# Kernel tuning notes

Measured on AMD Instinct MI355X. Metric: run time of the kernel, lower is better.

Reference implementation:

```python
import jax, jax.numpy as jnp
import numpy as np

B, S, D = 16, 4096, 1024
DIM_K, DIM_V, NUM_HEAD = 1024, 1024, 16


def setup_inputs() -> dict:
    key = jax.random.key(0)
    ks = jax.random.split(key, 7)
    s_in = 1.0 / np.sqrt(D)
    return {
        "x": jax.random.normal(ks[0], (B, S, D), dtype=jnp.float32),
        "Wq": jax.random.normal(ks[1], (D, DIM_K), dtype=jnp.float32) * s_in,
        "bq": jnp.zeros((DIM_K,), dtype=jnp.float32),
        "Wk": jax.random.normal(ks[2], (D, DIM_K), dtype=jnp.float32) * s_in,
        "bk": jnp.zeros((DIM_K,), dtype=jnp.float32),
        "Wv": jax.random.normal(ks[3], (D, DIM_V), dtype=jnp.float32) * s_in,
        "bv": jnp.zeros((DIM_V,), dtype=jnp.float32),
    }


def reference(x, Wq, bq, Wk, bk, Wv, bv):
    H = NUM_HEAD
    b, s, _ = x.shape
    Q = x @ Wq + bq                      # (B,S,dim_k)
    K = x @ Wk + bk                      # (B,S,dim_k)
    V = x @ Wv + bv                      # (B,S,dim_v)
    Q_ = Q.reshape(b, s, H, DIM_K // H)  # (B,S,H,dk)
    K_ = K.reshape(b, s, H, DIM_K // H)
    V_ = V.reshape(b, s, H, DIM_V // H)
    # NOTE: faithful to the source quirk — scores are across HEADS (H x H)
    # at each (batch, seq) position; no 1/sqrt(dim_k) scaling (unused in source).
    scores = jnp.einsum("bshd,bsgd->bshg", Q_, K_)   # (B,S,H,H)
    atten = jax.nn.softmax(scores, axis=-1)
    out = jnp.einsum("bshg,bsgd->bshd", atten, V_)    # (B,S,H,dv_head)
    return out.reshape(b, s, -1)                      # (B,S,dim_v)
```

## Files before the change

kernel.cpp:

```cpp
#include <hip/hip_runtime.h>
#include <stdint.h>

#define M_TOTAL 65536
#define DIM     1024
#define NQKV    3072
#define NHEAD   16
#define HDIM    64

typedef __attribute__((ext_vector_type(8))) _Float16 f16x8;
typedef __attribute__((ext_vector_type(4))) _Float16 f16x4;
typedef __attribute__((ext_vector_type(4))) float    f32x4;

__global__ __launch_bounds__(256) void cvt_x_kernel(const float* __restrict__ x,
                                                    _Float16* __restrict__ xh,
                                                    int n4) {
    int i = blockIdx.x * blockDim.x + threadIdx.x;
    int stride = gridDim.x * blockDim.x;
    const float4* x4 = (const float4*)x;
    f16x4* o4 = (f16x4*)xh;
    for (; i < n4; i += stride) {
        float4 v = x4[i];
        f16x4 o;
        o[0] = (_Float16)v.x; o[1] = (_Float16)v.y;
        o[2] = (_Float16)v.z; o[3] = (_Float16)v.w;
        o4[i] = o;
    }
}

__global__ void cvt_w_kernel(const float* __restrict__ Wq,
                             const float* __restrict__ Wk,
                             const float* __restrict__ Wv,
                             _Float16* __restrict__ Wt) {
    __shared__ float tile[32][33];
    int which = blockIdx.z;
    const float* W = (which == 0) ? Wq : (which == 1) ? Wk : Wv;
    int d0 = blockIdx.y * 32, n0 = blockIdx.x * 32;
    int tx = threadIdx.x, ty = threadIdx.y;
    tile[ty][tx] = W[(size_t)(d0 + ty) * DIM + n0 + tx];
    __syncthreads();
    Wt[(size_t)(which * DIM + n0 + ty) * DIM + d0 + tx] = (_Float16)tile[tx][ty];
}

__global__ __launch_bounds__(256) void bias_kernel(const float* __restrict__ bq,
                                                   const float* __restrict__ bk,
                                                   const float* __restrict__ bv,
                                                   float* __restrict__ bias) {
    int i = blockIdx.x * 256 + threadIdx.x;
    if (i < NQKV)
        bias[i] = (i < 1024) ? bq[i] : (i < 2048) ? bk[i - 1024] : bv[i - 2048];
}


#define LDSA(slot)  ((slot) << 15)
#define LDSB(slot)  (65536 + ((slot) << 15))

__global__ __launch_bounds__(512, 2) void qkv_gemm_kernel(const _Float16* __restrict__ Xh,
                                                          const _Float16* __restrict__ Wth,
                                                          const float* __restrict__ bias,
                                                          _Float16* __restrict__ Ch) {
    extern __shared__ char smem[];

    const int bid = blockIdx.x;
    const int swz = (bid & 7) * (3072 / 8) + (bid >> 3);
    const int tm  = swz / (NQKV / 256);
    const int tn  = swz % (NQKV / 256);
    const int brow = tm * 256;
    const int bcol = tn * 256;

    const int tid = threadIdx.x;
    const int w   = tid >> 6;
    const int l   = tid & 63;
    const int wm  = w >> 2;
    const int wn  = w & 3;

    const int lrow8 = l >> 3;
    const int lcol8 = (l & 7) ^ lrow8;
    const _Float16* pAsrc = Xh  + (size_t)(brow + w * 8 + lrow8) * DIM + lcol8 * 8;
    const _Float16* pBsrc = Wth + (size_t)(bcol + w * 8 + lrow8) * DIM + lcol8 * 8;

    auto stageA = [&](int slot, int kt) {
#pragma unroll
        for (int ln = 0; ln < 4; ++ln) {
            const _Float16* s = pAsrc + (size_t)(ln * 64) * DIM + ((size_t)kt << 6);
            char* d = smem + LDSA(slot) + ln * 8192 + (w << 10);
            __builtin_amdgcn_global_load_lds((const __attribute__((address_space(1))) void*)s,
                                             (__attribute__((address_space(3))) void*)d, 16, 0, 0);
        }
    };
    auto stageB = [&](int slot, int kt) {
#pragma unroll
        for (int ln = 0; ln < 4; ++ln) {
            const _Float16* s = pBsrc + (size_t)(ln * 64) * DIM + ((size_t)kt << 6);
            char* d = smem + LDSB(slot) + ln * 8192 + (w << 10);
            __builtin_amdgcn_global_load_lds((const __attribute__((address_space(1))) void*)s,
                                             (__attribute__((address_space(3))) void*)d, 16, 0, 0);
        }
    };

    const int aRowB = ((wm << 7) + (l & 15)) << 7;
    const int bRowB = 65536 + (((wn << 6) + (l & 15)) << 7);
    const int xk0 = (((l >> 4) ^ (l & 7)) << 4);
    const int xk1 = ((((l >> 4) + 4) ^ (l & 7)) << 4);
    auto LDA = [&](int slot, int mi, int ks) -> f16x8 {
        return *(const f16x8*)(smem + (slot << 15) + aRowB + (mi << 11) + (ks ? xk1 : xk0));
    };
    auto LDB = [&](int slot, int ni, int ks) -> f16x8 {
        return *(const f16x8*)(smem + (slot << 15) + bRowB + (ni << 11) + (ks ? xk1 : xk0));
    };

    f32x4 acc[8][4] = {};
    f16x8 a[8][2], b[4][2];

    auto READS = [&](int slot) {
#pragma unroll
        for (int mi = 0; mi < 8; ++mi) { a[mi][0] = LDA(slot, mi, 0); a[mi][1] = LDA(slot, mi, 1); }
#pragma unroll
        for (int ni = 0; ni < 4; ++ni) { b[ni][0] = LDB(slot, ni, 0); b[ni][1] = LDB(slot, ni, 1); }
    };

    stageA(0, 0); stageB(0, 0);
    stageA(1, 1); stageB(1, 1);
    asm volatile("s_waitcnt vmcnt(8)" ::: "memory");
    __builtin_amdgcn_s_barrier();
    __builtin_amdgcn_sched_barrier(0);
    READS(0);

#pragma unroll 1
    for (int u = 0; u < 16; ++u) {
        const int s = u & 1;

        __builtin_amdgcn_s_setprio(1);
#pragma unroll
        for (int mi = 0; mi < 8; ++mi)
#pragma unroll
            for (int ni = 0; ni < 4; ++ni) {
                acc[mi][ni] = __builtin_amdgcn_mfma_f32_16x16x32_f16(b[ni][0], a[mi][0], acc[mi][ni], 0, 0, 0);
                acc[mi][ni] = __builtin_amdgcn_mfma_f32_16x16x32_f16(b[ni][1], a[mi][1], acc[mi][ni], 0, 0, 0);
            }
        __builtin_amdgcn_s_setprio(0);

        asm volatile("s_waitcnt lgkmcnt(0)" ::: "memory");
        __builtin_amdgcn_sched_barrier(0);
        __builtin_amdgcn_s_barrier();
        __builtin_amdgcn_sched_barrier(0);

        int kt = u + 2; if (kt > 15) kt = 15;
        stageA(s, kt); stageB(s, kt);

        asm volatile("s_waitcnt vmcnt(8)" ::: "memory");
        __builtin_amdgcn_sched_barrier(0);
        __builtin_amdgcn_s_barrier();
        __builtin_amdgcn_sched_barrier(0);

        READS(1 - s);
    }

    __syncthreads();
#pragma unroll
    for (int mi = 0; mi < 8; ++mi) {
        const int m = (wm << 7) + (mi << 4) + (l & 15);
        const int msw = m & 7;
#pragma unroll
        for (int ni = 0; ni < 4; ++ni) {
            const int n0 = (wn << 6) + (ni << 4) + ((l >> 4) << 2);
            const float4 bv4 = *(const float4*)&bias[bcol + n0];
            f16x4 h;
            h[0] = (_Float16)(acc[mi][ni][0] + bv4.x);
            h[1] = (_Float16)(acc[mi][ni][1] + bv4.y);
            h[2] = (_Float16)(acc[mi][ni][2] + bv4.z);
            h[3] = (_Float16)(acc[mi][ni][3] + bv4.w);
            const int c8 = n0 >> 2;
            *(f16x4*)(smem + m * 512 + (((c8 >> 1) ^ msw) << 4) + ((c8 & 1) << 3)) = h;
        }
    }
    __syncthreads();
#pragma unroll
    for (int it = 0; it < 16; ++it) {
        const int row = (tid >> 5) + (it << 4);
        const int c16 = tid & 31;
        f16x8 vv = *(const f16x8*)(smem + row * 512 + ((c16 ^ (row & 7)) << 4));
        *(f16x8*)&Ch[(size_t)(brow + row) * NQKV + bcol + (c16 << 3)] = vv;
    }
}

__global__ __launch_bounds__(256) void attn_kernel(const _Float16* __restrict__ QKVh,
                                                   float* __restrict__ out) {
    __shared__ _Float16 vlds[4][1024];
    __shared__ float attlds[4][16][16];

    const int w = threadIdx.x >> 6, l = threadIdx.x & 63;
    const size_t p = (size_t)blockIdx.x * 4 + w;
    const _Float16* base = QKVh + p * NQKV;
    const _Float16* qrow = base;
    const _Float16* krow = base + 1024;
    const _Float16* vrow = base + 2048;
    const int h = l & 15;
    const int g4 = (l >> 4) * 4;

    *(uint4*)&vlds[w][l * 16]     = *(const uint4*)&vrow[l * 16];
    *(uint4*)&vlds[w][l * 16 + 8] = *(const uint4*)&vrow[l * 16 + 8];

    const int fo = (l & 15) * HDIM + (l >> 4) * 8;
    f16x8 aK0 = *(const f16x8*)&krow[fo];
    f16x8 aK1 = *(const f16x8*)&krow[fo + 32];
    f16x8 bQ0 = *(const f16x8*)&qrow[fo];
    f16x8 bQ1 = *(const f16x8*)&qrow[fo + 32];

    f32x4 sT = {0.f, 0.f, 0.f, 0.f};
    sT = __builtin_amdgcn_mfma_f32_16x16x32_f16(aK0, bQ0, sT, 0, 0, 0);
    sT = __builtin_amdgcn_mfma_f32_16x16x32_f16(aK1, bQ1, sT, 0, 0, 0);

    float m = fmaxf(fmaxf(sT[0], sT[1]), fmaxf(sT[2], sT[3]));
    m = fmaxf(m, __shfl_xor(m, 16));
    m = fmaxf(m, __shfl_xor(m, 32));
    float e0 = __expf(sT[0] - m), e1 = __expf(sT[1] - m);
    float e2 = __expf(sT[2] - m), e3 = __expf(sT[3] - m);
    float s = e0 + e1 + e2 + e3;
    s += __shfl_xor(s, 16);
    s += __shfl_xor(s, 32);
    const float inv = 1.0f / s;

    float4 att = make_float4(e0 * inv, e1 * inv, e2 * inv, e3 * inv);
    *(float4*)&attlds[w][h][g4] = att;
    __syncthreads();

    const int dbase = (l >> 4) * 16;
    float acc[16];
#pragma unroll
    for (int c = 0; c < 16; ++c) acc[c] = 0.f;

#pragma unroll
    for (int g = 0; g < 16; ++g) {
        const float av = attlds[w][h][g];
        f16x8 v0 = *(const f16x8*)&vlds[w][g * HDIM + dbase];
        f16x8 v1 = *(const f16x8*)&vlds[w][g * HDIM + dbase + 8];
#pragma unroll
        for (int c = 0; c < 8; ++c) {
            acc[c]     += av * (float)v0[c];
            acc[c + 8] += av * (float)v1[c];
        }
    }

    float* op = out + p * DIM + h * HDIM + dbase;
#pragma unroll
    for (int c = 0; c < 16; c += 4)
        *(float4*)(op + c) = make_float4(acc[c], acc[c + 1], acc[c + 2], acc[c + 3]);
}

extern "C" void kernel_launch(void* const* d_in, const int* in_sizes, int n_in,
                              void* d_out, int out_size, void* d_ws, size_t ws_size,
                              hipStream_t stream) {
    const float* x  = (const float*)d_in[0];
    const float* Wq = (const float*)d_in[1];
    const float* bq = (const float*)d_in[2];
    const float* Wk = (const float*)d_in[3];
    const float* bk = (const float*)d_in[4];
    const float* Wv = (const float*)d_in[5];
    const float* bv = (const float*)d_in[6];
    float* out = (float*)d_out;

    char* ws = (char*)d_ws;
    _Float16* Xh  = (_Float16*)ws;
    _Float16* Wth = (_Float16*)(ws + 134217728);
    float*    bias = (float*)(ws + 134217728 + 6291456);
    _Float16* Ch  = (_Float16*)(ws + 134217728 + 6291456 + 12288);

    (void)hipFuncSetAttribute((const void*)qkv_gemm_kernel,
                              hipFuncAttributeMaxDynamicSharedMemorySize, 131072);

    hipLaunchKernelGGL(cvt_x_kernel, dim3(2048), dim3(256), 0, stream,
                       x, Xh, (M_TOTAL * DIM) / 4);
    hipLaunchKernelGGL(cvt_w_kernel, dim3(32, 32, 3), dim3(32, 32), 0, stream,
                       Wq, Wk, Wv, Wth);
    hipLaunchKernelGGL(bias_kernel, dim3(12), dim3(256), 0, stream,
                       bq, bk, bv, bias);
    hipLaunchKernelGGL(qkv_gemm_kernel, dim3((M_TOTAL / 256) * (NQKV / 256)), dim3(512), 131072, stream,
                       Xh, Wth, bias, Ch);
    hipLaunchKernelGGL(attn_kernel, dim3(M_TOTAL / 4), dim3(256), 0, stream,
                       Ch, out);
}
```

Baseline: 675.7 us.

## Interleave LDS fragment reads with MFMA quadrants in QKV GEMM main loop

Splits the per-k-tile register fragments into four quadrants and interleaves LDS reads of the next quadrant with MFMA on the current one, using fine-grained lgkmcnt waits. The global-to-LDS staging for tile u+2 is issued midway through compute, and the last two k-tiles are peeled out of the loop so no redundant stage is issued. The aim is to hide LDS read latency behind MFMA work and cut register pressure from holding full fragments. In exchange it adds hand-tuned wait counts that must match the compiler's instruction order exactly.

```diff
diff --git a/kernel.cpp b/kernel.cpp
--- a/kernel.cpp
+++ b/kernel.cpp
@@ -54,6 +54,20 @@
 #define LDSA(slot)  ((slot) << 15)
 #define LDSB(slot)  (65536 + ((slot) << 15))
 
+#define MFMA16(AF, BF, MB, NB)                                                  \
+    __builtin_amdgcn_s_setprio(1);                                              \
+    _Pragma("unroll") for (int mi = 0; mi < 4; ++mi)                            \
+    _Pragma("unroll") for (int ni = 0; ni < 2; ++ni)                            \
+    _Pragma("unroll") for (int ks = 0; ks < 2; ++ks)                            \
+        acc[(MB) + mi][(NB) + ni] = __builtin_amdgcn_mfma_f32_16x16x32_f16(     \
+            BF[ni][ks], AF[mi][ks], acc[(MB) + mi][(NB) + ni], 0, 0, 0);        \
+    __builtin_amdgcn_s_setprio(0);
+
+#define LGKM(n)  do { asm volatile("s_waitcnt lgkmcnt(" #n ")" ::: "memory");   \
+                      __builtin_amdgcn_sched_barrier(0); } while (0)
+#define VMCNT(n) do { asm volatile("s_waitcnt vmcnt(" #n ")" ::: "memory");     \
+                      __builtin_amdgcn_sched_barrier(0); } while (0)
+
 __global__ __launch_bounds__(512, 2) void qkv_gemm_kernel(const _Float16* __restrict__ Xh,
                                                           const _Float16* __restrict__ Wth,
                                                           const float* __restrict__ bias,
@@ -109,51 +123,60 @@
     };
 
     f32x4 acc[8][4] = {};
-    f16x8 a[8][2], b[4][2];
-
-    auto READS = [&](int slot) {
-#pragma unroll
-        for (int mi = 0; mi < 8; ++mi) { a[mi][0] = LDA(slot, mi, 0); a[mi][1] = LDA(slot, mi, 1); }
-#pragma unroll
-        for (int ni = 0; ni < 4; ++ni) { b[ni][0] = LDB(slot, ni, 0); b[ni][1] = LDB(slot, ni, 1); }
+    f16x8 aA[4][2], aB[4][2], bA[2][2], bB[2][2];
+
+    auto READ_A0 = [&](int slot) {
+#pragma unroll
+        for (int mi = 0; mi < 4; ++mi) { aA[mi][0] = LDA(slot, mi, 0); aA[mi][1] = LDA(slot, mi, 1); }
+    };
+    auto READ_A4 = [&](int slot) {
+#pragma unroll
+        for (int mi = 0; mi < 4; ++mi) { aB[mi][0] = LDA(slot, mi + 4, 0); aB[mi][1] = LDA(slot, mi + 4, 1); }
+    };
+    auto READ_B0 = [&](int slot) {
+#pragma unroll
+        for (int ni = 0; ni < 2; ++ni) { bA[ni][0] = LDB(slot, ni, 0); bA[ni][1] = LDB(slot, ni, 1); }
+    };
+    auto READ_B2 = [&](int slot) {
+#pragma unroll
+        for (int ni = 0; ni < 2; ++ni) { bB[ni][0] = LDB(slot, ni + 2, 0); bB[ni][1] = LDB(slot, ni + 2, 1); }
     };
 
     stageA(0, 0); stageB(0, 0);
     stageA(1, 1); stageB(1, 1);
-    asm volatile("s_waitcnt vmcnt(8)" ::: "memory");
+    VMCNT(8);
     __builtin_amdgcn_s_barrier();
-    __builtin_amdgcn_sched_barrier(0);
-    READS(0);
+    READ_A0(0); READ_B0(0);
 
 #pragma unroll 1
-    for (int u = 0; u < 16; ++u) {
+    for (int u = 0; u < 14; ++u) {
         const int s = u & 1;
-
-        __builtin_amdgcn_s_setprio(1);
-#pragma unroll
-        for (int mi = 0; mi < 8; ++mi)
-#pragma unroll
-            for (int ni = 0; ni < 4; ++ni) {
-                acc[mi][ni] = __builtin_amdgcn_mfma_f32_16x16x32_f16(b[ni][0], a[mi][0], acc[mi][ni], 0, 0, 0);
-                acc[mi][ni] = __builtin_amdgcn_mfma_f32_16x16x32_f16(b[ni][1], a[mi][1], acc[mi][ni], 0, 0, 0);
-            }
-        __builtin_amdgcn_s_setprio(0);
-
-        asm volatile("s_waitcnt lgkmcnt(0)" ::: "memory");
-        __builtin_amdgcn_sched_barrier(0);
+        READ_B2(s);  LGKM(4);  MFMA16(aA, bA, 0, 0)
+        READ_A4(s);  LGKM(8);  MFMA16(aA, bB, 0, 2)
+        READ_B0(s);  LGKM(4);  MFMA16(aB, bB, 4, 2)
+        LGKM(0);
         __builtin_amdgcn_s_barrier();
-        __builtin_amdgcn_sched_barrier(0);
-
-        int kt = u + 2; if (kt > 15) kt = 15;
-        stageA(s, kt); stageB(s, kt);
-
-        asm volatile("s_waitcnt vmcnt(8)" ::: "memory");
-        __builtin_amdgcn_sched_barrier(0);
+        stageA(s, u + 2); stageB(s, u + 2);
+        MFMA16(aB, bA, 4, 0)
+        VMCNT(8);
         __builtin_amdgcn_s_barrier();
-        __builtin_amdgcn_sched_barrier(0);
-
-        READS(1 - s);
-    }
+        READ_A0(1 - s); READ_B0(1 - s);
+    }
+
+    READ_B2(0);  LGKM(4);  MFMA16(aA, bA, 0, 0)
+    READ_A4(0);  LGKM(8);  MFMA16(aA, bB, 0, 2)
+    READ_B0(0);  LGKM(4);  MFMA16(aB, bB, 4, 2)
+    LGKM(0);
+    MFMA16(aB, bA, 4, 0)
+    VMCNT(0);
+    __builtin_amdgcn_s_barrier();
+    READ_A0(1); READ_B0(1);
+
+    READ_B2(1);  LGKM(4);  MFMA16(aA, bA, 0, 0)
+    READ_A4(1);  LGKM(8);  MFMA16(aA, bB, 0, 2)
+    READ_B0(1);  LGKM(4);  MFMA16(aB, bB, 4, 2)
+    LGKM(0);
+    MFMA16(aB, bA, 4, 0)
 
     __syncthreads();
 #pragma unroll
```

Measured after the change: 646.7 us. -4.3%, faster.
